# Kernel optimization log

Measured on AMD Instinct MI355X. Metric: run time of the kernel, lower is better.

The kernel has to match this reference:

```python
import jax, jax.numpy as jnp
import numpy as np

N, B, H, OUT, T = 200000, 1024, 256, 128, 2  # nodes, graphs, hidden(=in_dim), out_dim, timesteps
NEG_SLOPE = 0.01


def setup_inputs() -> dict:
    key = jax.random.key(0)
    ks = jax.random.split(key, 12)
    s = 0.05
    f32 = jnp.float32
    return {
        "x": jax.random.normal(ks[0], (N, H), dtype=f32),
        "batch": jnp.sort(jax.random.randint(ks[1], (N,), 0, B)),
        # GATConv params (heads=1, shared lin for src/dst since in_channels is int)
        "W": jax.random.normal(ks[2], (H, H), dtype=f32) * s,
        "att_src": jax.random.normal(ks[3], (H,), dtype=f32) * s,
        "att_dst": jax.random.normal(ks[4], (H,), dtype=f32) * s,
        "bias_gat": jnp.zeros((H,), dtype=f32),
        # GRUCell params (input_size = H, hidden_size = H)
        "W_ih": jax.random.normal(ks[5], (3 * H, H), dtype=f32) * s,
        "W_hh": jax.random.normal(ks[6], (3 * H, H), dtype=f32) * s,
        "b_ih": jnp.zeros((3 * H,), dtype=f32),
        "b_hh": jnp.zeros((3 * H,), dtype=f32),
        # final Linear
        "W_lin": jax.random.normal(ks[7], (H, OUT), dtype=f32) * s,
        "b_lin": jnp.zeros((OUT,), dtype=f32),
    }


def reference(x, batch, W, att_src, att_dst, bias_gat, W_ih, W_hh, b_ih, b_hh, W_lin, b_lin):
    # out = global_add_pool(x, batch)  -> [B, H]
    out = jax.ops.segment_sum(x, batch, num_segments=B)
    for _ in range(T):
        # --- bipartite GATConv((x, out), edge_index=[arange(N), batch]) ---
        xs = x @ W                       # [N, H] transformed source nodes
        od = out @ W                     # [B, H] transformed dst (graph) nodes
        a_src = xs @ att_src             # [N]
        a_dst = od @ att_dst             # [B]
        e = a_src + a_dst[batch]         # [N] per-edge raw score (one edge per node)
        e = jnp.where(e > 0, e, NEG_SLOPE * e)  # leaky_relu(negative_slope=0.01)
        # scatter-softmax over each graph's incoming edges
        emax = jax.ops.segment_max(e, batch, num_segments=B)
        ee = jnp.exp(e - emax[batch])
        denom = jax.ops.segment_sum(ee, batch, num_segments=B)
        alpha = ee / denom[batch]        # [N]
        # scatter-add aggregation of weighted messages
        agg = jax.ops.segment_sum(xs * alpha[:, None], batch, num_segments=B) + bias_gat
        h = jax.nn.elu(agg)              # [B, H]  (dropout is identity in eval)
        # --- GRUCell(h, out) ---
        gi = h @ W_ih.T + b_ih           # [B, 3H]
        gh = out @ W_hh.T + b_hh         # [B, 3H]
        r = jax.nn.sigmoid(gi[:, :H] + gh[:, :H])
        z = jax.nn.sigmoid(gi[:, H:2 * H] + gh[:, H:2 * H])
        n = jnp.tanh(gi[:, 2 * H:] + r * gh[:, 2 * H:])
        out = jax.nn.silu((1.0 - z) * n + z * out)  # activation = F.silu
    return out @ W_lin + b_lin           # [B, OUT]
```

## Files before the change

### kernel.cpp

```cpp
#include <hip/hip_runtime.h>
#include <math.h>

#define N_NODES 200000
#define BGRAPH  1024
#define HDIM    256
#define ODIM    128
#define TSTEPS  2

#define ACT_NONE 0
#define ACT_ELU  1

__global__ void k_vectors(const float* __restrict__ W, const float* __restrict__ att_src,
                          const float* __restrict__ att_dst, float* __restrict__ v,
                          float* __restrict__ u) {
    int i = threadIdx.x;
    float sv = 0.f, su = 0.f;
    for (int j = 0; j < HDIM; ++j) {
        float w = W[i * HDIM + j];
        sv += w * att_src[j];
        su += w * att_dst[j];
    }
    v[i] = sv; u[i] = su;
}

__global__ void k_bounds(const int* __restrict__ batch, int* __restrict__ seg) {
    int b = blockIdx.x * blockDim.x + threadIdx.x;
    if (b > BGRAPH) return;
    if (b == BGRAPH) { seg[b] = N_NODES; return; }
    int lo = 0, hi = N_NODES;
    while (lo < hi) { int mid = (lo + hi) >> 1; if (batch[mid] < b) lo = mid + 1; else hi = mid; }
    seg[b] = lo;
}

__global__ __launch_bounds__(256) void k_passA(const float* __restrict__ x,
        const int* __restrict__ seg, const float* __restrict__ v,
        float* __restrict__ s, float* __restrict__ stt) {
    int b = blockIdx.x;
    int lo = seg[b], hi = seg[b + 1];
    int t = threadIdx.x, wave = t >> 6, lane = t & 63;
    float v0 = v[4 * lane + 0], v1 = v[4 * lane + 1], v2 = v[4 * lane + 2], v3 = v[4 * lane + 3];
    float p0 = 0.f, p1 = 0.f, p2 = 0.f, p3 = 0.f;
    int i = lo + wave;
    for (; i + 4 < hi; i += 8) {
        const float4 r0 = *(const float4*)(x + (size_t)i * HDIM + 4 * lane);
        const float4 r1 = *(const float4*)(x + (size_t)(i + 4) * HDIM + 4 * lane);
        p0 += r0.x + r1.x; p1 += r0.y + r1.y; p2 += r0.z + r1.z; p3 += r0.w + r1.w;
        float pa = r0.x * v0 + r0.y * v1 + r0.z * v2 + r0.w * v3;
        float pb = r1.x * v0 + r1.y * v1 + r1.z * v2 + r1.w * v3;
        #pragma unroll
        for (int off = 32; off > 0; off >>= 1) {
            pa += __shfl_down(pa, off, 64);
            pb += __shfl_down(pb, off, 64);
        }
        if (lane == 0) { s[i] = pa; s[i + 4] = pb; }
    }
    for (; i < hi; i += 4) {
        const float4 r0 = *(const float4*)(x + (size_t)i * HDIM + 4 * lane);
        p0 += r0.x; p1 += r0.y; p2 += r0.z; p3 += r0.w;
        float pa = r0.x * v0 + r0.y * v1 + r0.z * v2 + r0.w * v3;
        #pragma unroll
        for (int off = 32; off > 0; off >>= 1) pa += __shfl_down(pa, off, 64);
        if (lane == 0) s[i] = pa;
    }
    __shared__ float comb[4][HDIM];
    comb[wave][4 * lane + 0] = p0; comb[wave][4 * lane + 1] = p1;
    comb[wave][4 * lane + 2] = p2; comb[wave][4 * lane + 3] = p3;
    __syncthreads();
    stt[(size_t)b * HDIM + t] = comb[0][t] + comb[1][t] + comb[2][t] + comb[3][t];
}

__global__ __launch_bounds__(256) void k_iter_h(const float* __restrict__ x,
        const int* __restrict__ seg, const float* __restrict__ s,
        const float* __restrict__ u, const float* __restrict__ stt,
        const float* __restrict__ W, const float* __restrict__ bias_gat,
        float* __restrict__ hbuf) {
    int b = blockIdx.x, t = threadIdx.x;
    int lo = seg[b], hi = seg[b + 1];
    __shared__ float red[256];
    red[t] = stt[(size_t)b * HDIM + t] * u[t];
    __syncthreads();
    for (int st = 128; st > 0; st >>= 1) { if (t < st) red[t] += red[t + st]; __syncthreads(); }
    float d = red[0];
    __syncthreads();
    float m = -3.402823466e38f;
    for (int i = lo + t; i < hi; i += 256) {
        float e = s[i] + d; e = e > 0.f ? e : 0.01f * e;
        m = fmaxf(m, e);
    }
    red[t] = m; __syncthreads();
    for (int st = 128; st > 0; st >>= 1) { if (t < st) red[t] = fmaxf(red[t], red[t + st]); __syncthreads(); }
    float M = red[0];
    __syncthreads();
    float sm = 0.f;
    for (int i = lo + t; i < hi; i += 256) {
        float e = s[i] + d; e = e > 0.f ? e : 0.01f * e;
        sm += __expf(e - M);
    }
    red[t] = sm; __syncthreads();
    for (int st = 128; st > 0; st >>= 1) { if (t < st) red[t] += red[t + st]; __syncthreads(); }
    float inv = (hi > lo) ? 1.0f / red[0] : 0.f;
    __syncthreads();
    int wave = t >> 6, lane = t & 63;
    float a0 = 0.f, a1 = 0.f, a2 = 0.f, a3 = 0.f;
    int i = lo + wave;
    for (; i + 4 < hi; i += 8) {
        float e0 = s[i] + d;     e0 = e0 > 0.f ? e0 : 0.01f * e0;
        float e1 = s[i + 4] + d; e1 = e1 > 0.f ? e1 : 0.01f * e1;
        float al0 = __expf(e0 - M) * inv;
        float al1 = __expf(e1 - M) * inv;
        const float4 r0 = *(const float4*)(x + (size_t)i * HDIM + 4 * lane);
        const float4 r1 = *(const float4*)(x + (size_t)(i + 4) * HDIM + 4 * lane);
        a0 += al0 * r0.x + al1 * r1.x; a1 += al0 * r0.y + al1 * r1.y;
        a2 += al0 * r0.z + al1 * r1.z; a3 += al0 * r0.w + al1 * r1.w;
    }
    for (; i < hi; i += 4) {
        float e0 = s[i] + d; e0 = e0 > 0.f ? e0 : 0.01f * e0;
        float al0 = __expf(e0 - M) * inv;
        const float4 r0 = *(const float4*)(x + (size_t)i * HDIM + 4 * lane);
        a0 += al0 * r0.x; a1 += al0 * r0.y; a2 += al0 * r0.z; a3 += al0 * r0.w;
    }
    __shared__ float comb[4][HDIM];
    comb[wave][4 * lane + 0] = a0; comb[wave][4 * lane + 1] = a1;
    comb[wave][4 * lane + 2] = a2; comb[wave][4 * lane + 3] = a3;
    __syncthreads();
    __shared__ float ax[HDIM];
    ax[t] = comb[0][t] + comb[1][t] + comb[2][t] + comb[3][t];
    __syncthreads();
    float acc = bias_gat[t];
    #pragma unroll 8
    for (int ii = 0; ii < HDIM; ++ii) acc += ax[ii] * W[(size_t)ii * HDIM + t];
    hbuf[(size_t)b * HDIM + t] = acc > 0.f ? acc : expm1f(acc);
}

__global__ __launch_bounds__(256) void k_gemm2(const float* __restrict__ A0,
        const float* __restrict__ A1, const float* __restrict__ B0,
        const float* __restrict__ B1, float* __restrict__ C0, float* __restrict__ C1,
        int M, int N, int K) {
    const float* A = blockIdx.z ? A1 : A0;
    const float* B = blockIdx.z ? B1 : B0;
    float* C = blockIdx.z ? C1 : C0;
    __shared__ __align__(16) float As[16][64];
    __shared__ __align__(16) float Bs[16][64];
    int tx = threadIdx.x & 15, ty = threadIdx.x >> 4;
    int m0 = blockIdx.x * 64, n0 = blockIdx.y * 64;
    float acc[4][4] = {};
    for (int k0 = 0; k0 < K; k0 += 16) {
        {
            int r = threadIdx.x >> 2;
            int kk = (threadIdx.x & 3) << 2;
            float4 av = *(const float4*)(A + (size_t)(m0 + r) * K + k0 + kk);
            As[kk + 0][r] = av.x; As[kk + 1][r] = av.y;
            As[kk + 2][r] = av.z; As[kk + 3][r] = av.w;
            float4 bv = *(const float4*)(B + (size_t)(n0 + r) * K + k0 + kk);
            Bs[kk + 0][r] = bv.x; Bs[kk + 1][r] = bv.y;
            Bs[kk + 2][r] = bv.z; Bs[kk + 3][r] = bv.w;
        }
        __syncthreads();
        #pragma unroll
        for (int kk = 0; kk < 16; ++kk) {
            float4 a = *(const float4*)&As[kk][ty * 4];
            float4 bb = *(const float4*)&Bs[kk][tx * 4];
            acc[0][0] += a.x * bb.x; acc[0][1] += a.x * bb.y; acc[0][2] += a.x * bb.z; acc[0][3] += a.x * bb.w;
            acc[1][0] += a.y * bb.x; acc[1][1] += a.y * bb.y; acc[1][2] += a.y * bb.z; acc[1][3] += a.y * bb.w;
            acc[2][0] += a.z * bb.x; acc[2][1] += a.z * bb.y; acc[2][2] += a.z * bb.z; acc[2][3] += a.z * bb.w;
            acc[3][0] += a.w * bb.x; acc[3][1] += a.w * bb.y; acc[3][2] += a.w * bb.z; acc[3][3] += a.w * bb.w;
        }
        __syncthreads();
    }
    #pragma unroll
    for (int i = 0; i < 4; ++i) {
        int mrow = m0 + ty * 4 + i;
        *(float4*)(C + (size_t)mrow * N + n0 + tx * 4) =
            make_float4(acc[i][0], acc[i][1], acc[i][2], acc[i][3]);
    }
}

__global__ __launch_bounds__(256) void k_gemm_nn(const float* __restrict__ A,
        const float* __restrict__ B, const float* __restrict__ bias,
        float* __restrict__ C, int M, int N, int K) {
    __shared__ __align__(16) float As[16][64];
    __shared__ __align__(16) float Bs[16][64];
    int tx = threadIdx.x & 15, ty = threadIdx.x >> 4;
    int m0 = blockIdx.x * 64, n0 = blockIdx.y * 64;
    float acc[4][4] = {};
    for (int k0 = 0; k0 < K; k0 += 16) {
        {
            int r = threadIdx.x >> 2;
            int kk = (threadIdx.x & 3) << 2;
            float4 av = *(const float4*)(A + (size_t)(m0 + r) * K + k0 + kk);
            As[kk + 0][r] = av.x; As[kk + 1][r] = av.y;
            As[kk + 2][r] = av.z; As[kk + 3][r] = av.w;
        }
        {
            int kk = threadIdx.x >> 4;
            int nn = (threadIdx.x & 15) << 2;
            float4 bv = *(const float4*)(B + (size_t)(k0 + kk) * N + n0 + nn);
            Bs[kk][nn + 0] = bv.x; Bs[kk][nn + 1] = bv.y;
            Bs[kk][nn + 2] = bv.z; Bs[kk][nn + 3] = bv.w;
        }
        __syncthreads();
        #pragma unroll
        for (int kk = 0; kk < 16; ++kk) {
            float4 a = *(const float4*)&As[kk][ty * 4];
            float4 bb = *(const float4*)&Bs[kk][tx * 4];
            acc[0][0] += a.x * bb.x; acc[0][1] += a.x * bb.y; acc[0][2] += a.x * bb.z; acc[0][3] += a.x * bb.w;
            acc[1][0] += a.y * bb.x; acc[1][1] += a.y * bb.y; acc[1][2] += a.y * bb.z; acc[1][3] += a.y * bb.w;
            acc[2][0] += a.z * bb.x; acc[2][1] += a.z * bb.y; acc[2][2] += a.z * bb.z; acc[2][3] += a.z * bb.w;
            acc[3][0] += a.w * bb.x; acc[3][1] += a.w * bb.y; acc[3][2] += a.w * bb.z; acc[3][3] += a.w * bb.w;
        }
        __syncthreads();
    }
    float bsv[4];
    #pragma unroll
    for (int j = 0; j < 4; ++j) bsv[j] = bias[n0 + tx * 4 + j];
    #pragma unroll
    for (int i = 0; i < 4; ++i) {
        int mrow = m0 + ty * 4 + i;
        *(float4*)(C + (size_t)mrow * N + n0 + tx * 4) =
            make_float4(acc[i][0] + bsv[0], acc[i][1] + bsv[1],
                        acc[i][2] + bsv[2], acc[i][3] + bsv[3]);
    }
}

__global__ __launch_bounds__(256) void k_gru(const float* __restrict__ gi,
        const float* __restrict__ gh, const float* __restrict__ b_ih,
        const float* __restrict__ b_hh, float* __restrict__ stt) {
    int idx = blockIdx.x * 256 + threadIdx.x;
    int j = idx & 255;
    size_t base = (size_t)(idx >> 8) * (3 * HDIM);
    float gir = gi[base + j] + b_ih[j];
    float giz = gi[base + HDIM + j] + b_ih[HDIM + j];
    float gin = gi[base + 2 * HDIM + j] + b_ih[2 * HDIM + j];
    float ghr = gh[base + j] + b_hh[j];
    float ghz = gh[base + HDIM + j] + b_hh[HDIM + j];
    float ghn = gh[base + 2 * HDIM + j] + b_hh[2 * HDIM + j];
    float r = 1.f / (1.f + __expf(-(gir + ghr)));
    float z = 1.f / (1.f + __expf(-(giz + ghz)));
    float n = tanhf(gin + r * ghn);
    float prev = stt[idx];
    float h2 = (1.f - z) * n + z * prev;
    stt[idx] = h2 / (1.f + __expf(-h2));
}

extern "C" void kernel_launch(void* const* d_in, const int* in_sizes, int n_in,
                              void* d_out, int out_size, void* d_ws, size_t ws_size,
                              hipStream_t stream) {
    const float* x        = (const float*)d_in[0];
    const int*   batch    = (const int*)d_in[1];
    const float* W        = (const float*)d_in[2];
    const float* att_src  = (const float*)d_in[3];
    const float* att_dst  = (const float*)d_in[4];
    const float* bias_gat = (const float*)d_in[5];
    const float* W_ih     = (const float*)d_in[6];
    const float* W_hh     = (const float*)d_in[7];
    const float* b_ih     = (const float*)d_in[8];
    const float* b_hh     = (const float*)d_in[9];
    const float* W_lin    = (const float*)d_in[10];
    const float* b_lin    = (const float*)d_in[11];

    char* ws = (char*)d_ws;
    size_t off = 0;
    auto alloc = [&](size_t bytes) {
        void* p = (void*)(ws + off);
        off += (bytes + 255) & ~(size_t)255;
        return p;
    };
    float* s    = (float*)alloc((size_t)N_NODES * 4);
    int*   seg  = (int*)alloc((BGRAPH + 1) * 4);
    float* vv   = (float*)alloc(HDIM * 4);
    float* uu   = (float*)alloc(HDIM * 4);
    float* stt  = (float*)alloc((size_t)BGRAPH * HDIM * 4);
    float* hbuf = (float*)alloc((size_t)BGRAPH * HDIM * 4);
    float* gi   = (float*)alloc((size_t)BGRAPH * 3 * HDIM * 4);
    float* gh   = (float*)alloc((size_t)BGRAPH * 3 * HDIM * 4);

    hipLaunchKernelGGL(k_vectors, dim3(1), dim3(HDIM), 0, stream, W, att_src, att_dst, vv, uu);
    hipLaunchKernelGGL(k_bounds, dim3(5), dim3(256), 0, stream, batch, seg);
    hipLaunchKernelGGL(k_passA, dim3(BGRAPH), dim3(256), 0, stream, x, seg, vv, s, stt);

    for (int tstep = 0; tstep < TSTEPS; ++tstep) {
        hipLaunchKernelGGL(k_iter_h, dim3(BGRAPH), dim3(256), 0, stream,
                           x, seg, s, uu, stt, W, bias_gat, hbuf);
        hipLaunchKernelGGL(k_gemm2, dim3(BGRAPH / 64, (3 * HDIM) / 64, 2), dim3(256), 0,
                           stream, hbuf, stt, W_ih, W_hh, gi, gh, BGRAPH, 3 * HDIM, HDIM);
        hipLaunchKernelGGL(k_gru, dim3(BGRAPH * HDIM / 256), dim3(256), 0, stream,
                           gi, gh, b_ih, b_hh, stt);
    }
    hipLaunchKernelGGL(k_gemm_nn, dim3(BGRAPH / 64, ODIM / 64), dim3(256), 0,
                       stream, stt, W_lin, b_lin, (float*)d_out, BGRAPH, ODIM, HDIM);
}
```

Measured before the change: 484.2 us.

## Fuse softmax passes, drop per-node score buffer, fuse GRU into neighbouring kernels

Computes the segment max of attention scores analytically from the per-graph max of x·v (leaky_relu is monotonic), so iter_h does a single pass that recomputes scores, accumulates weighted sums and the denominator together. The per-node score buffer is removed, the GRU elementwise step is fused into the next iter_h and into the final linear kernel, and the prep kernels are merged. Node loops are unrolled to four rows per wave for more loads in flight. This trades extra dot-product and shuffle work per row and redundant GRU recomputation in the final GEMM for fewer passes, syncs and launches.

```diff
diff --git a/kernel.cpp b/kernel.cpp
--- a/kernel.cpp
+++ b/kernel.cpp
@@ -7,124 +7,172 @@
 #define ODIM    128
 #define TSTEPS  2
 
-#define ACT_NONE 0
-#define ACT_ELU  1
-
-__global__ void k_vectors(const float* __restrict__ W, const float* __restrict__ att_src,
-                          const float* __restrict__ att_dst, float* __restrict__ v,
-                          float* __restrict__ u) {
-    int i = threadIdx.x;
-    float sv = 0.f, su = 0.f;
-    for (int j = 0; j < HDIM; ++j) {
-        float w = W[i * HDIM + j];
-        sv += w * att_src[j];
-        su += w * att_dst[j];
-    }
-    v[i] = sv; u[i] = su;
-}
-
-__global__ void k_bounds(const int* __restrict__ batch, int* __restrict__ seg) {
-    int b = blockIdx.x * blockDim.x + threadIdx.x;
-    if (b > BGRAPH) return;
-    if (b == BGRAPH) { seg[b] = N_NODES; return; }
-    int lo = 0, hi = N_NODES;
-    while (lo < hi) { int mid = (lo + hi) >> 1; if (batch[mid] < b) lo = mid + 1; else hi = mid; }
-    seg[b] = lo;
+__global__ __launch_bounds__(256) void k_prep(const float* __restrict__ W,
+        const float* __restrict__ att_src, const float* __restrict__ att_dst,
+        const int* __restrict__ batch, float* __restrict__ v, float* __restrict__ u,
+        int* __restrict__ seg) {
+    int t = threadIdx.x;
+    if (blockIdx.x < 256) {
+        int i = blockIdx.x;
+        float w = W[(size_t)i * HDIM + t];
+        __shared__ float r1[256], r2[256];
+        r1[t] = w * att_src[t];
+        r2[t] = w * att_dst[t];
+        __syncthreads();
+        for (int st = 128; st > 0; st >>= 1) {
+            if (t < st) { r1[t] += r1[t + st]; r2[t] += r2[t + st]; }
+            __syncthreads();
+        }
+        if (t == 0) { v[i] = r1[0]; u[i] = r2[0]; }
+    } else {
+        int b = (blockIdx.x - 256) * 256 + t;
+        if (b > BGRAPH) return;
+        if (b == BGRAPH) { seg[b] = N_NODES; return; }
+        int lo = 0, hi = N_NODES;
+        while (lo < hi) { int mid = (lo + hi) >> 1; if (batch[mid] < b) lo = mid + 1; else hi = mid; }
+        seg[b] = lo;
+    }
 }
 
 __global__ __launch_bounds__(256) void k_passA(const float* __restrict__ x,
         const int* __restrict__ seg, const float* __restrict__ v,
-        float* __restrict__ s, float* __restrict__ stt) {
+        float* __restrict__ stt, float* __restrict__ smax) {
     int b = blockIdx.x;
     int lo = seg[b], hi = seg[b + 1];
     int t = threadIdx.x, wave = t >> 6, lane = t & 63;
     float v0 = v[4 * lane + 0], v1 = v[4 * lane + 1], v2 = v[4 * lane + 2], v3 = v[4 * lane + 3];
     float p0 = 0.f, p1 = 0.f, p2 = 0.f, p3 = 0.f;
+    float sm = -3.402823466e38f;
     int i = lo + wave;
-    for (; i + 4 < hi; i += 8) {
+    for (; i + 12 < hi; i += 16) {
         const float4 r0 = *(const float4*)(x + (size_t)i * HDIM + 4 * lane);
         const float4 r1 = *(const float4*)(x + (size_t)(i + 4) * HDIM + 4 * lane);
-        p0 += r0.x + r1.x; p1 += r0.y + r1.y; p2 += r0.z + r1.z; p3 += r0.w + r1.w;
-        float pa = r0.x * v0 + r0.y * v1 + r0.z * v2 + r0.w * v3;
-        float pb = r1.x * v0 + r1.y * v1 + r1.z * v2 + r1.w * v3;
-        #pragma unroll
-        for (int off = 32; off > 0; off >>= 1) {
-            pa += __shfl_down(pa, off, 64);
-            pb += __shfl_down(pb, off, 64);
-        }
-        if (lane == 0) { s[i] = pa; s[i + 4] = pb; }
+        const float4 r2 = *(const float4*)(x + (size_t)(i + 8) * HDIM + 4 * lane);
+        const float4 r3 = *(const float4*)(x + (size_t)(i + 12) * HDIM + 4 * lane);
+        p0 += r0.x + r1.x + r2.x + r3.x; p1 += r0.y + r1.y + r2.y + r3.y;
+        p2 += r0.z + r1.z + r2.z + r3.z; p3 += r0.w + r1.w + r2.w + r3.w;
+        float d0 = r0.x * v0 + r0.y * v1 + r0.z * v2 + r0.w * v3;
+        float d1 = r1.x * v0 + r1.y * v1 + r1.z * v2 + r1.w * v3;
+        float d2 = r2.x * v0 + r2.y * v1 + r2.z * v2 + r2.w * v3;
+        float d3 = r3.x * v0 + r3.y * v1 + r3.z * v2 + r3.w * v3;
+        #pragma unroll
+        for (int off = 1; off < 64; off <<= 1) {
+            d0 += __shfl_xor(d0, off, 64);
+            d1 += __shfl_xor(d1, off, 64);
+            d2 += __shfl_xor(d2, off, 64);
+            d3 += __shfl_xor(d3, off, 64);
+        }
+        sm = fmaxf(sm, fmaxf(fmaxf(d0, d1), fmaxf(d2, d3)));
     }
     for (; i < hi; i += 4) {
         const float4 r0 = *(const float4*)(x + (size_t)i * HDIM + 4 * lane);
         p0 += r0.x; p1 += r0.y; p2 += r0.z; p3 += r0.w;
-        float pa = r0.x * v0 + r0.y * v1 + r0.z * v2 + r0.w * v3;
-        #pragma unroll
-        for (int off = 32; off > 0; off >>= 1) pa += __shfl_down(pa, off, 64);
-        if (lane == 0) s[i] = pa;
+        float d0 = r0.x * v0 + r0.y * v1 + r0.z * v2 + r0.w * v3;
+        #pragma unroll
+        for (int off = 1; off < 64; off <<= 1) d0 += __shfl_xor(d0, off, 64);
+        sm = fmaxf(sm, d0);
     }
     __shared__ float comb[4][HDIM];
     comb[wave][4 * lane + 0] = p0; comb[wave][4 * lane + 1] = p1;
     comb[wave][4 * lane + 2] = p2; comb[wave][4 * lane + 3] = p3;
+    __shared__ float sred[4];
+    if (lane == 0) sred[wave] = sm;
     __syncthreads();
     stt[(size_t)b * HDIM + t] = comb[0][t] + comb[1][t] + comb[2][t] + comb[3][t];
-}
-
+    if (t == 0) smax[b] = fmaxf(fmaxf(sred[0], sred[1]), fmaxf(sred[2], sred[3]));
+}
+
+template<int DO_GRU>
 __global__ __launch_bounds__(256) void k_iter_h(const float* __restrict__ x,
-        const int* __restrict__ seg, const float* __restrict__ s,
-        const float* __restrict__ u, const float* __restrict__ stt,
+        const int* __restrict__ seg, const float* __restrict__ v,
+        const float* __restrict__ u, const float* __restrict__ smax,
+        float* __restrict__ stt,
+        const float* __restrict__ gi, const float* __restrict__ gh,
+        const float* __restrict__ b_ih, const float* __restrict__ b_hh,
         const float* __restrict__ W, const float* __restrict__ bias_gat,
         float* __restrict__ hbuf) {
     int b = blockIdx.x, t = threadIdx.x;
     int lo = seg[b], hi = seg[b + 1];
+    float st_j;
+    if (DO_GRU) {
+        size_t base = (size_t)b * (3 * HDIM);
+        float gir = gi[base + t] + b_ih[t];
+        float giz = gi[base + HDIM + t] + b_ih[HDIM + t];
+        float gin = gi[base + 2 * HDIM + t] + b_ih[2 * HDIM + t];
+        float ghr = gh[base + t] + b_hh[t];
+        float ghz = gh[base + HDIM + t] + b_hh[HDIM + t];
+        float ghn = gh[base + 2 * HDIM + t] + b_hh[2 * HDIM + t];
+        float r = 1.f / (1.f + __expf(-(gir + ghr)));
+        float z = 1.f / (1.f + __expf(-(giz + ghz)));
+        float n = tanhf(gin + r * ghn);
+        float prev = stt[(size_t)b * HDIM + t];
+        float h2 = (1.f - z) * n + z * prev;
+        st_j = h2 / (1.f + __expf(-h2));
+        stt[(size_t)b * HDIM + t] = st_j;
+    } else {
+        st_j = stt[(size_t)b * HDIM + t];
+    }
     __shared__ float red[256];
-    red[t] = stt[(size_t)b * HDIM + t] * u[t];
+    red[t] = st_j * u[t];
     __syncthreads();
     for (int st = 128; st > 0; st >>= 1) { if (t < st) red[t] += red[t + st]; __syncthreads(); }
-    float d = red[0];
-    __syncthreads();
-    float m = -3.402823466e38f;
-    for (int i = lo + t; i < hi; i += 256) {
-        float e = s[i] + d; e = e > 0.f ? e : 0.01f * e;
-        m = fmaxf(m, e);
-    }
-    red[t] = m; __syncthreads();
-    for (int st = 128; st > 0; st >>= 1) { if (t < st) red[t] = fmaxf(red[t], red[t + st]); __syncthreads(); }
-    float M = red[0];
-    __syncthreads();
-    float sm = 0.f;
-    for (int i = lo + t; i < hi; i += 256) {
-        float e = s[i] + d; e = e > 0.f ? e : 0.01f * e;
-        sm += __expf(e - M);
-    }
-    red[t] = sm; __syncthreads();
-    for (int st = 128; st > 0; st >>= 1) { if (t < st) red[t] += red[t + st]; __syncthreads(); }
-    float inv = (hi > lo) ? 1.0f / red[0] : 0.f;
-    __syncthreads();
+    float datt = red[0];
+    __syncthreads();
+    float M = smax[b] + datt;
+    M = M > 0.f ? M : 0.01f * M;
+
     int wave = t >> 6, lane = t & 63;
-    float a0 = 0.f, a1 = 0.f, a2 = 0.f, a3 = 0.f;
+    float v0 = v[4 * lane + 0], v1 = v[4 * lane + 1], v2 = v[4 * lane + 2], v3 = v[4 * lane + 3];
+    float a0 = 0.f, a1 = 0.f, a2 = 0.f, a3 = 0.f, den = 0.f;
     int i = lo + wave;
-    for (; i + 4 < hi; i += 8) {
-        float e0 = s[i] + d;     e0 = e0 > 0.f ? e0 : 0.01f * e0;
-        float e1 = s[i + 4] + d; e1 = e1 > 0.f ? e1 : 0.01f * e1;
-        float al0 = __expf(e0 - M) * inv;
-        float al1 = __expf(e1 - M) * inv;
+    for (; i + 12 < hi; i += 16) {
         const float4 r0 = *(const float4*)(x + (size_t)i * HDIM + 4 * lane);
         const float4 r1 = *(const float4*)(x + (size_t)(i + 4) * HDIM + 4 * lane);
-        a0 += al0 * r0.x + al1 * r1.x; a1 += al0 * r0.y + al1 * r1.y;
-        a2 += al0 * r0.z + al1 * r1.z; a3 += al0 * r0.w + al1 * r1.w;
+        const float4 r2 = *(const float4*)(x + (size_t)(i + 8) * HDIM + 4 * lane);
+        const float4 r3 = *(const float4*)(x + (size_t)(i + 12) * HDIM + 4 * lane);
+        float d0 = r0.x * v0 + r0.y * v1 + r0.z * v2 + r0.w * v3;
+        float d1 = r1.x * v0 + r1.y * v1 + r1.z * v2 + r1.w * v3;
+        float d2 = r2.x * v0 + r2.y * v1 + r2.z * v2 + r2.w * v3;
+        float d3 = r3.x * v0 + r3.y * v1 + r3.z * v2 + r3.w * v3;
+        #pragma unroll
+        for (int off = 1; off < 64; off <<= 1) {
+            d0 += __shfl_xor(d0, off, 64);
+            d1 += __shfl_xor(d1, off, 64);
+            d2 += __shfl_xor(d2, off, 64);
+            d3 += __shfl_xor(d3, off, 64);
+        }
+        float e0 = d0 + datt; e0 = e0 > 0.f ? e0 : 0.01f * e0;
+        float e1 = d1 + datt; e1 = e1 > 0.f ? e1 : 0.01f * e1;
+        float e2 = d2 + datt; e2 = e2 > 0.f ? e2 : 0.01f * e2;
+        float e3 = d3 + datt; e3 = e3 > 0.f ? e3 : 0.01f * e3;
+        float w0 = __expf(e0 - M), w1 = __expf(e1 - M);
+        float w2 = __expf(e2 - M), w3 = __expf(e3 - M);
+        den += (w0 + w1) + (w2 + w3);
+        a0 += w0 * r0.x + w1 * r1.x + w2 * r2.x + w3 * r3.x;
+        a1 += w0 * r0.y + w1 * r1.y + w2 * r2.y + w3 * r3.y;
+        a2 += w0 * r0.z + w1 * r1.z + w2 * r2.z + w3 * r3.z;
+        a3 += w0 * r0.w + w1 * r1.w + w2 * r2.w + w3 * r3.w;
     }
     for (; i < hi; i += 4) {
-        float e0 = s[i] + d; e0 = e0 > 0.f ? e0 : 0.01f * e0;
-        float al0 = __expf(e0 - M) * inv;
         const float4 r0 = *(const float4*)(x + (size_t)i * HDIM + 4 * lane);
-        a0 += al0 * r0.x; a1 += al0 * r0.y; a2 += al0 * r0.z; a3 += al0 * r0.w;
+        float d0 = r0.x * v0 + r0.y * v1 + r0.z * v2 + r0.w * v3;
+        #pragma unroll
+        for (int off = 1; off < 64; off <<= 1) d0 += __shfl_xor(d0, off, 64);
+        float e0 = d0 + datt; e0 = e0 > 0.f ? e0 : 0.01f * e0;
+        float w0 = __expf(e0 - M);
+        den += w0;
+        a0 += w0 * r0.x; a1 += w0 * r0.y; a2 += w0 * r0.z; a3 += w0 * r0.w;
     }
     __shared__ float comb[4][HDIM];
+    __shared__ float dred[4];
     comb[wave][4 * lane + 0] = a0; comb[wave][4 * lane + 1] = a1;
     comb[wave][4 * lane + 2] = a2; comb[wave][4 * lane + 3] = a3;
-    __syncthreads();
+    if (lane == 0) dred[wave] = den;
+    __syncthreads();
+    float dtot = dred[0] + dred[1] + dred[2] + dred[3];
+    float inv = (hi > lo) ? 1.0f / dtot : 0.f;
     __shared__ float ax[HDIM];
-    ax[t] = comb[0][t] + comb[1][t] + comb[2][t] + comb[3][t];
+    ax[t] = (comb[0][t] + comb[1][t] + comb[2][t] + comb[3][t]) * inv;
     __syncthreads();
     float acc = bias_gat[t];
     #pragma unroll 8
@@ -175,7 +223,9 @@
     }
 }
 
-__global__ __launch_bounds__(256) void k_gemm_nn(const float* __restrict__ A,
+__global__ __launch_bounds__(256) void k_final(const float* __restrict__ gi,
+        const float* __restrict__ gh, const float* __restrict__ b_ih,
+        const float* __restrict__ b_hh, const float* __restrict__ stt,
         const float* __restrict__ B, const float* __restrict__ bias,
         float* __restrict__ C, int M, int N, int K) {
     __shared__ __align__(16) float As[16][64];
@@ -186,10 +236,25 @@
     for (int k0 = 0; k0 < K; k0 += 16) {
         {
             int r = threadIdx.x >> 2;
-            int kk = (threadIdx.x & 3) << 2;
-            float4 av = *(const float4*)(A + (size_t)(m0 + r) * K + k0 + kk);
-            As[kk + 0][r] = av.x; As[kk + 1][r] = av.y;
-            As[kk + 2][r] = av.z; As[kk + 3][r] = av.w;
+            int kk0 = (threadIdx.x & 3) << 2;
+            int mrow = m0 + r;
+            size_t base = (size_t)mrow * (3 * HDIM);
+            #pragma unroll
+            for (int q = 0; q < 4; ++q) {
+                int k = k0 + kk0 + q;
+                float gir = gi[base + k] + b_ih[k];
+                float giz = gi[base + HDIM + k] + b_ih[HDIM + k];
+                float gin = gi[base + 2 * HDIM + k] + b_ih[2 * HDIM + k];
+                float ghr = gh[base + k] + b_hh[k];
+                float ghz = gh[base + HDIM + k] + b_hh[HDIM + k];
+                float ghn = gh[base + 2 * HDIM + k] + b_hh[2 * HDIM + k];
+                float rg = 1.f / (1.f + __expf(-(gir + ghr)));
+                float zg = 1.f / (1.f + __expf(-(giz + ghz)));
+                float ng = tanhf(gin + rg * ghn);
+                float prev = stt[(size_t)mrow * HDIM + k];
+                float h2 = (1.f - zg) * ng + zg * prev;
+                As[kk0 + q][r] = h2 / (1.f + __expf(-h2));
+            }
         }
         {
             int kk = threadIdx.x >> 4;
@@ -220,26 +285,6 @@
             make_float4(acc[i][0] + bsv[0], acc[i][1] + bsv[1],
                         acc[i][2] + bsv[2], acc[i][3] + bsv[3]);
     }
-}
-
-__global__ __launch_bounds__(256) void k_gru(const float* __restrict__ gi,
-        const float* __restrict__ gh, const float* __restrict__ b_ih,
-        const float* __restrict__ b_hh, float* __restrict__ stt) {
-    int idx = blockIdx.x * 256 + threadIdx.x;
-    int j = idx & 255;
-    size_t base = (size_t)(idx >> 8) * (3 * HDIM);
-    float gir = gi[base + j] + b_ih[j];
-    float giz = gi[base + HDIM + j] + b_ih[HDIM + j];
-    float gin = gi[base + 2 * HDIM + j] + b_ih[2 * HDIM + j];
-    float ghr = gh[base + j] + b_hh[j];
-    float ghz = gh[base + HDIM + j] + b_hh[HDIM + j];
-    float ghn = gh[base + 2 * HDIM + j] + b_hh[2 * HDIM + j];
-    float r = 1.f / (1.f + __expf(-(gir + ghr)));
-    float z = 1.f / (1.f + __expf(-(giz + ghz)));
-    float n = tanhf(gin + r * ghn);
-    float prev = stt[idx];
-    float h2 = (1.f - z) * n + z * prev;
-    stt[idx] = h2 / (1.f + __expf(-h2));
 }
 
 extern "C" void kernel_launch(void* const* d_in, const int* in_sizes, int n_in,
@@ -265,27 +310,30 @@
         off += (bytes + 255) & ~(size_t)255;
         return p;
     };
-    float* s    = (float*)alloc((size_t)N_NODES * 4);
     int*   seg  = (int*)alloc((BGRAPH + 1) * 4);
     float* vv   = (float*)alloc(HDIM * 4);
     float* uu   = (float*)alloc(HDIM * 4);
+    float* smax = (float*)alloc(BGRAPH * 4);
     float* stt  = (float*)alloc((size_t)BGRAPH * HDIM * 4);
     float* hbuf = (float*)alloc((size_t)BGRAPH * HDIM * 4);
     float* gi   = (float*)alloc((size_t)BGRAPH * 3 * HDIM * 4);
     float* gh   = (float*)alloc((size_t)BGRAPH * 3 * HDIM * 4);
 
-    hipLaunchKernelGGL(k_vectors, dim3(1), dim3(HDIM), 0, stream, W, att_src, att_dst, vv, uu);
-    hipLaunchKernelGGL(k_bounds, dim3(5), dim3(256), 0, stream, batch, seg);
-    hipLaunchKernelGGL(k_passA, dim3(BGRAPH), dim3(256), 0, stream, x, seg, vv, s, stt);
-
-    for (int tstep = 0; tstep < TSTEPS; ++tstep) {
-        hipLaunchKernelGGL(k_iter_h, dim3(BGRAPH), dim3(256), 0, stream,
-                           x, seg, s, uu, stt, W, bias_gat, hbuf);
-        hipLaunchKernelGGL(k_gemm2, dim3(BGRAPH / 64, (3 * HDIM) / 64, 2), dim3(256), 0,
-                           stream, hbuf, stt, W_ih, W_hh, gi, gh, BGRAPH, 3 * HDIM, HDIM);
-        hipLaunchKernelGGL(k_gru, dim3(BGRAPH * HDIM / 256), dim3(256), 0, stream,
-                           gi, gh, b_ih, b_hh, stt);
-    }
-    hipLaunchKernelGGL(k_gemm_nn, dim3(BGRAPH / 64, ODIM / 64), dim3(256), 0,
-                       stream, stt, W_lin, b_lin, (float*)d_out, BGRAPH, ODIM, HDIM);
-}
+    hipLaunchKernelGGL(k_prep, dim3(261), dim3(256), 0, stream,
+                       W, att_src, att_dst, batch, vv, uu, seg);
+    hipLaunchKernelGGL(k_passA, dim3(BGRAPH), dim3(256), 0, stream, x, seg, vv, stt, smax);
+
+    hipLaunchKernelGGL((k_iter_h<0>), dim3(BGRAPH), dim3(256), 0, stream,
+                       x, seg, vv, uu, smax, stt, (const float*)nullptr, (const float*)nullptr,
+                       b_ih, b_hh, W, bias_gat, hbuf);
+    hipLaunchKernelGGL(k_gemm2, dim3(BGRAPH / 64, (3 * HDIM) / 64, 2), dim3(256), 0,
+                       stream, hbuf, stt, W_ih, W_hh, gi, gh, BGRAPH, 3 * HDIM, HDIM);
+    hipLaunchKernelGGL((k_iter_h<1>), dim3(BGRAPH), dim3(256), 0, stream,
+                       x, seg, vv, uu, smax, stt, gi, gh,
+                       b_ih, b_hh, W, bias_gat, hbuf);
+    hipLaunchKernelGGL(k_gemm2, dim3(BGRAPH / 64, (3 * HDIM) / 64, 2), dim3(256), 0,
+                       stream, hbuf, stt, W_ih, W_hh, gi, gh, BGRAPH, 3 * HDIM, HDIM);
+    hipLaunchKernelGGL(k_final, dim3(BGRAPH / 64, ODIM / 64), dim3(256), 0, stream,
+                       gi, gh, b_ih, b_hh, stt, W_lin, b_lin, (float*)d_out,
+                       BGRAPH, ODIM, HDIM);
+}
```

New measurement: 518.0 us. 7.0% more time.
